# Kernel optimization log

Hardware: AMD Instinct MI355X
Metric: run time of the kernel (lower is better)

Reference implementation:

```python
import jax, jax.numpy as jnp
import numpy as np


def _conv1x1(x, W, b):
    # x: (n, c_in, h, w); W: (c_out, c_in); b: (c_out,)
    return jnp.einsum('nchw,oc->nohw', x, W) + b[None, :, None, None]


def setup_inputs() -> dict:
    key = jax.random.key(0)
    ks = jax.random.split(key, 9)
    n, C, h, w = 2, 256, 64, 64
    Ch = C // 2
    s_in = 0.02
    return {
        'feature': jax.random.normal(ks[0], (n, C, h, w), dtype=jnp.float32),
        'Wq': jax.random.normal(ks[1], (Ch, C), dtype=jnp.float32) * s_in,
        'bq': jax.random.normal(ks[2], (Ch,), dtype=jnp.float32) * s_in,
        'Wk': jax.random.normal(ks[3], (Ch, C), dtype=jnp.float32) * s_in,
        'bk': jax.random.normal(ks[4], (Ch,), dtype=jnp.float32) * s_in,
        'Wv': jax.random.normal(ks[5], (Ch, C), dtype=jnp.float32) * s_in,
        'bv': jax.random.normal(ks[6], (Ch,), dtype=jnp.float32) * s_in,
        'Wm': jax.random.normal(ks[7], (C, Ch), dtype=jnp.float32) * s_in,
        'bm': jax.random.normal(ks[8], (C,), dtype=jnp.float32) * s_in,
    }


def reference(feature, Wq, bq, Wk, bk, Wv, bv, Wm, bm):
    n, C, h, w = feature.shape
    Ch = C // 2
    N = n * h * w
    # 1x1 conv projections, then flatten batch+spatial into one sequence dim
    q = _conv1x1(feature, Wq, bq)  # (n, Ch, h, w)
    k = _conv1x1(feature, Wk, bk)
    v = _conv1x1(feature, Wv, bv)
    # NCHW -> NHWC -> (N, Ch), matching torch transpose(1,2).transpose(2,3).reshape
    q = jnp.transpose(q, (0, 2, 3, 1)).reshape(N, Ch)
    k = jnp.transpose(k, (0, 2, 3, 1)).reshape(N, Ch)
    v = jnp.transpose(v, (0, 2, 3, 1)).reshape(N, Ch)
    # scores = k @ q.T (note: torch code uses k as rows, q.T as cols)
    scores = k @ q.T  # (N, N)
    attn = jax.nn.softmax(scores, axis=-1)
    mask = attn @ v  # (N, Ch)
    mask = mask.reshape(n, h, w, Ch)
    # torch transpose chain (2,3)->(1,2)->(2,3): (n,h,w,Ch) -> (n,Ch,w,h)
    mask = jnp.transpose(mask, (0, 3, 2, 1))
    out = _conv1x1(mask, Wm, bm)  # (n, C, w, h); h==w so residual add is valid
    return out + feature
```

## Files before the change

kernel.cpp:

```cpp
#include <hip/hip_runtime.h>
#include <hip/hip_bf16.h>

#define LOG2E 1.44269504088896340736f

typedef __attribute__((ext_vector_type(8))) short short8;
typedef __attribute__((ext_vector_type(4))) float f32x4;
typedef __attribute__((ext_vector_type(2))) unsigned int uint2v;
typedef __attribute__((ext_vector_type(4))) unsigned int uint4v;
typedef unsigned int u32;

__device__ __forceinline__ short f2bf(float f) {
    unsigned u = __builtin_bit_cast(unsigned, f);
    unsigned r = (u + 0x7FFFu + ((u >> 16) & 1u)) >> 16;
    return (short)r;
}

__device__ __forceinline__ float bf2f(short x) {
    unsigned u = ((unsigned)(unsigned short)x) << 16;
    return __builtin_bit_cast(float, u);
}

__device__ __forceinline__ unsigned cvt_pk_bf16(float lo, float hi) {
    unsigned r;
    asm volatile("v_cvt_pk_bf16_f32 %0, %1, %2" : "=v"(r) : "v"(lo), "v"(hi));
    return r;
}

__device__ __forceinline__ float fexp2(float x) {
    float r;
    asm("v_exp_f32 %0, %1" : "=v"(r) : "v"(x));
    return r;
}

__global__ __launch_bounds__(64) void wprep_kernel(
    const float* __restrict__ Wq, const float* __restrict__ bq,
    const float* __restrict__ Wk, const float* __restrict__ bk,
    const float* __restrict__ Wv, const float* __restrict__ bv,
    const float* __restrict__ Wm,
    short* __restrict__ Wb, float* __restrict__ bqkv, short* __restrict__ Wmb)
{
    const int b = blockIdx.x;
    const int t = threadIdx.x;
    if (b < 384) {
        const int mat = b >> 7, row = b & 127;
        const float* src = (mat == 0 ? Wq : mat == 1 ? Wk : Wv) + (size_t)row * 256;
        const float sc = (mat == 1) ? LOG2E : 1.f;
        float4 v = *(const float4*)(src + t * 4);
        uint2v pk;
        pk.x = cvt_pk_bf16(v.x * sc, v.y * sc);
        pk.y = cvt_pk_bf16(v.z * sc, v.w * sc);
        *(uint2v*)(Wb + (size_t)b * 256 + t * 4) = pk;
    } else if (b == 384) {
        for (int e = t; e < 384; e += 64) {
            const int mat = e >> 7;
            const float* bsrc = (mat == 0 ? bq : mat == 1 ? bk : bv);
            bqkv[e] = bsrc[e & 127] * (mat == 1 ? LOG2E : 1.f);
        }
    } else {
        const int row = b - 385;
        float2 v = *(const float2*)(Wm + (size_t)row * 128 + t * 2);
        *(u32*)(Wmb + (size_t)row * 128 + t * 2) = cvt_pk_bf16(v.x, v.y);
    }
}

__global__ __launch_bounds__(256) void proj_kernel(
    const float* __restrict__ feat, const short* __restrict__ Wb,
    const float* __restrict__ bqkv,
    short* __restrict__ Qb, short* __restrict__ Kb, short* __restrict__ VTp)
{
    __shared__ __align__(16) short Xs[16 * 256];
    __shared__ __align__(16) short VTs[128 * 16];
    const int t = threadIdx.x;
    const int blk = blockIdx.x;
    const int ib = blk * 16;
    const int n = ib >> 12;
    const int hw0 = ib & 4095;

    {
        const int r = t & 15, cg = t >> 4;
        const float* fp = feat + (size_t)n * 1048576 + (size_t)(cg * 16) * 4096 + hw0 + r;
        short8 t0, t1;
        #pragma unroll
        for (int ci = 0; ci < 8; ++ci) {
            t0[ci] = f2bf(fp[(size_t)ci * 4096]);
            t1[ci] = f2bf(fp[(size_t)(ci + 8) * 4096]);
        }
        const int sw = (r & 7) << 2;
        *(short8*)(&Xs[r * 256 + ((cg * 2) ^ sw) * 8]) = t0;
        *(short8*)(&Xs[r * 256 + ((cg * 2 + 1) ^ sw) * 8]) = t1;
    }
    __syncthreads();

    const int lane = t & 63;
    const int w = __builtin_amdgcn_readfirstlane(t >> 6);
    const int l15 = lane & 15;
    const int g = lane >> 4;
    const int o0w = w * 96;

    f32x4 acc[6];
    #pragma unroll
    for (int osub = 0; osub < 6; ++osub)
        acc[osub] = *(const f32x4*)(bqkv + o0w + osub * 16 + 4 * g);

    const short* wbase = Wb + (size_t)(o0w + l15) * 256 + g * 8;
    const int xsw = (l15 & 7) << 2;
    #pragma unroll
    for (int kc = 0; kc < 8; ++kc) {
        short8 xf = *(const short8*)(&Xs[l15 * 256 + (((kc * 4 + g) ^ xsw) * 8)]);
        #pragma unroll
        for (int osub = 0; osub < 6; ++osub) {
            short8 wf = *(const short8*)(wbase + (size_t)osub * 16 * 256 + kc * 32);
            acc[osub] = __builtin_amdgcn_mfma_f32_16x16x32_bf16(wf, xf, acc[osub], 0, 0, 0);
        }
    }

    #pragma unroll
    for (int osub = 0; osub < 6; ++osub) {
        const int o0 = o0w + osub * 16;
        const int mat = o0 >> 7;
        const int col = (o0 & 127) + 4 * g;
        if (mat == 0) {
            uint2v pk;
            pk.x = cvt_pk_bf16(acc[osub][0], acc[osub][1]);
            pk.y = cvt_pk_bf16(acc[osub][2], acc[osub][3]);
            *(uint2v*)(Qb + (size_t)(ib + l15) * 128 + col) = pk;
        } else if (mat == 1) {
            uint2v pk;
            pk.x = cvt_pk_bf16(acc[osub][0], acc[osub][1]);
            pk.y = cvt_pk_bf16(acc[osub][2], acc[osub][3]);
            *(uint2v*)(Kb + (size_t)(ib + l15) * 128 + col) = pk;
        } else {
            #pragma unroll
            for (int reg = 0; reg < 4; ++reg)
                VTs[(col + reg) * 16 + l15] = f2bf(acc[osub][reg]);
        }
    }
    __syncthreads();

    {
        const int o = t >> 1, ih = (t & 1) * 8;
        short8 vv = *(const short8*)(&VTs[o * 16 + ih]);
        const int base32 = ib & ~31;
        const int u = (ib >> 4) & 1;
        const int p0 = 2 * ih + 4 * u;
        uint4v q = __builtin_bit_cast(uint4v, vv);
        uint2v lo; lo.x = q.x; lo.y = q.y;
        uint2v hi; hi.x = q.z; hi.y = q.w;
        *(uint2v*)(VTp + (size_t)o * 8192 + base32 + p0) = lo;
        *(uint2v*)(VTp + (size_t)o * 8192 + base32 + p0 + 8) = hi;
    }
}

__global__ __launch_bounds__(256, 2) void attn_kernel(
    const short* __restrict__ Qb, const short* __restrict__ Kb,
    const short* __restrict__ VTp,
    short* __restrict__ Opart, float* __restrict__ Ssb)
{
    __shared__ __align__(16) char smem[65536];

    const int tid = threadIdx.x;
    const int lane = tid & 63;
    const int w = __builtin_amdgcn_readfirstlane(tid >> 6);
    const int l15 = lane & 15;
    const int g = lane >> 4;
    const int blk = blockIdx.x;
    const int ibX = blk >> 3;
    const int jq  = blk & 7;
    const int iw  = ibX * 128 + w * 32;
    const int j0  = jq * 1024;

    short8 kf[2][4];
    #pragma unroll
    for (int iset = 0; iset < 2; ++iset)
        #pragma unroll
        for (int dcq = 0; dcq < 4; ++dcq)
            kf[iset][dcq] = *(const short8*)(Kb + (size_t)(iw + iset * 16 + l15) * 128 + dcq * 32 + g * 8);

    f32x4 O[2][8];
    #pragma unroll
    for (int iset = 0; iset < 2; ++iset)
        #pragma unroll
        for (int dc = 0; dc < 8; ++dc) O[iset][dc] = (f32x4){0.f, 0.f, 0.f, 0.f};
    float s[2] = {0.f, 0.f};

    const short* srcQ0;
    const short* srcQ1;
    const short* srcV0;
    const short* srcV1;
    {
        int r0 = 4 * w + (lane >> 4), c0 = lane & 15;
        srcQ0 = Qb + (size_t)(j0 + r0) * 128 + (c0 ^ (r0 & 7)) * 8;
        int r1 = 16 + 4 * w + (lane >> 4);
        srcQ1 = Qb + (size_t)(j0 + r1) * 128 + (c0 ^ (r1 & 7)) * 8;
        int d0 = 16 * w + (lane >> 2), c2 = lane & 3;
        srcV0 = VTp + (size_t)d0 * 8192 + j0 + (c2 ^ ((d0 >> 1) & 3)) * 8;
        int d1 = 64 + 16 * w + (lane >> 2);
        srcV1 = VTp + (size_t)d1 * 8192 + j0 + (c2 ^ ((d1 >> 1) & 3)) * 8;
    }

    auto stage = [&](int quarter) {
        char* base = smem + quarter * 16384;
        __builtin_amdgcn_global_load_lds(
            (const __attribute__((address_space(1))) u32*)(const void*)srcQ0,
            (__attribute__((address_space(3))) u32*)(void*)(base + w * 1024), 16, 0, 0);
        __builtin_amdgcn_global_load_lds(
            (const __attribute__((address_space(1))) u32*)(const void*)srcQ1,
            (__attribute__((address_space(3))) u32*)(void*)(base + (4 + w) * 1024), 16, 0, 0);
        __builtin_amdgcn_global_load_lds(
            (const __attribute__((address_space(1))) u32*)(const void*)srcV0,
            (__attribute__((address_space(3))) u32*)(void*)(base + (8 + w) * 1024), 16, 0, 0);
        __builtin_amdgcn_global_load_lds(
            (const __attribute__((address_space(1))) u32*)(const void*)srcV1,
            (__attribute__((address_space(3))) u32*)(void*)(base + (12 + w) * 1024), 16, 0, 0);
        srcQ0 += 32 * 128;
        srcQ1 += 32 * 128;
        srcV0 += 32;
        srcV1 += 32;
    };

    auto compute32 = [&](const char* base) {
        const char* Qt = base;
        const char* Vt = base + 8192;
        const int xs = (l15 & 7) << 4;

        f32x4 sv[2][2];
        #pragma unroll
        for (int jh = 0; jh < 2; ++jh)
            #pragma unroll
            for (int iset = 0; iset < 2; ++iset)
                sv[jh][iset] = (f32x4){-16.f, -16.f, -16.f, -16.f};

        __builtin_amdgcn_s_setprio(1);
        #pragma unroll
        for (int dcq = 0; dcq < 4; ++dcq) {
            short8 qa0 = *(const short8*)(Qt + ((l15 * 256 + dcq * 64 + g * 16) ^ xs));
            short8 qa1 = *(const short8*)(Qt + (((l15 + 16) * 256 + dcq * 64 + g * 16) ^ xs));
            sv[0][0] = __builtin_amdgcn_mfma_f32_16x16x32_bf16(qa0, kf[0][dcq], sv[0][0], 0, 0, 0);
            sv[0][1] = __builtin_amdgcn_mfma_f32_16x16x32_bf16(qa0, kf[1][dcq], sv[0][1], 0, 0, 0);
            sv[1][0] = __builtin_amdgcn_mfma_f32_16x16x32_bf16(qa1, kf[0][dcq], sv[1][0], 0, 0, 0);
            sv[1][1] = __builtin_amdgcn_mfma_f32_16x16x32_bf16(qa1, kf[1][dcq], sv[1][1], 0, 0, 0);
        }
        __builtin_amdgcn_s_setprio(0);

        short8 pf[2];
        #pragma unroll
        for (int iset = 0; iset < 2; ++iset) {
            float p0[4], p1[4], ps = 0.f;
            #pragma unroll
            for (int e = 0; e < 4; ++e) {
                p0[e] = fexp2(sv[0][iset][e]);
                p1[e] = fexp2(sv[1][iset][e]);
                ps += p0[e] + p1[e];
            }
            s[iset] += ps;
            uint4v pk;
            pk.x = cvt_pk_bf16(p0[0], p0[1]);
            pk.y = cvt_pk_bf16(p0[2], p0[3]);
            pk.z = cvt_pk_bf16(p1[0], p1[1]);
            pk.w = cvt_pk_bf16(p1[2], p1[3]);
            pf[iset] = __builtin_bit_cast(short8, pk);
        }

        __builtin_amdgcn_s_setprio(1);
        #pragma unroll
        for (int dc = 0; dc < 8; ++dc) {
            short8 va = *(const short8*)(Vt + (dc * 16 + l15) * 64 + ((g ^ ((l15 >> 1) & 3)) << 4));
            O[0][dc] = __builtin_amdgcn_mfma_f32_16x16x32_bf16(va, pf[0], O[0][dc], 0, 0, 0);
            O[1][dc] = __builtin_amdgcn_mfma_f32_16x16x32_bf16(va, pf[1], O[1][dc], 0, 0, 0);
        }
        __builtin_amdgcn_s_setprio(0);
    };

    stage(0);
    stage(1);
    __syncthreads();
    for (int tt = 0; tt < 32; tt += 2) {
        if (tt + 2 < 32) {
            stage((tt + 2) & 3);
            stage((tt + 3) & 3);
        }
        compute32(smem + (tt & 3) * 16384);
        compute32(smem + ((tt + 1) & 3) * 16384);
        __syncthreads();
    }

    #pragma unroll
    for (int iset = 0; iset < 2; ++iset) {
        const int i = iw + iset * 16 + l15;
        #pragma unroll
        for (int dc = 0; dc < 8; ++dc) {
            uint2v pk;
            pk.x = cvt_pk_bf16(O[iset][dc][0], O[iset][dc][1]);
            pk.y = cvt_pk_bf16(O[iset][dc][2], O[iset][dc][3]);
            *(uint2v*)(Opart + ((size_t)i * 8 + jq) * 128 + dc * 16 + 4 * g) = pk;
        }
        Ssb[(i * 8 + jq) * 4 + g] = s[iset];
    }
}

__global__ __launch_bounds__(256, 4) void epi_kernel(
    const short* __restrict__ Opart, const float* __restrict__ Ssb,
    const short* __restrict__ Wmb, const float* __restrict__ bm,
    const float* __restrict__ feat, float* __restrict__ out)
{
    __shared__ __align__(16) short Ms[16 * 128];
    const int t = threadIdx.x;
    const int blk = blockIdx.x;
    const int yt = blk & 3;
    const int x = (blk >> 2) & 63;
    const int n = blk >> 8;
    const int y0 = yt * 16;

    {
        const int r = t >> 4, c = t & 15;
        const int i = n * 4096 + (y0 + r) * 64 + x;
        float acc8[8] = {0.f, 0.f, 0.f, 0.f, 0.f, 0.f, 0.f, 0.f};
        #pragma unroll
        for (int q = 0; q < 8; ++q) {
            short8 o = *(const short8*)(Opart + ((size_t)i * 8 + q) * 128 + c * 8);
            #pragma unroll
            for (int e = 0; e < 8; ++e) acc8[e] += bf2f(o[e]);
        }
        float2 s2 = *(const float2*)(Ssb + (size_t)i * 32 + c * 2);
        float tp = s2.x + s2.y;
        tp += __shfl_xor(tp, 1);
        tp += __shfl_xor(tp, 2);
        tp += __shfl_xor(tp, 4);
        tp += __shfl_xor(tp, 8);
        const float inv = 1.f / tp;
        uint4v pk;
        pk.x = cvt_pk_bf16(acc8[0] * inv, acc8[1] * inv);
        pk.y = cvt_pk_bf16(acc8[2] * inv, acc8[3] * inv);
        pk.z = cvt_pk_bf16(acc8[4] * inv, acc8[5] * inv);
        pk.w = cvt_pk_bf16(acc8[6] * inv, acc8[7] * inv);
        *(short8*)(&Ms[r * 128 + ((c ^ ((r & 7) << 1)) * 8)]) =
            __builtin_bit_cast(short8, pk);
    }
    __syncthreads();

    const int lane = t & 63;
    const int w = __builtin_amdgcn_readfirstlane(t >> 6);
    const int l15 = lane & 15;
    const int g = lane >> 4;
    const int c0 = w * 64;

    short8 bf[4];
    const int msw = (l15 & 7) << 1;
    #pragma unroll
    for (int dcq = 0; dcq < 4; ++dcq)
        bf[dcq] = *(const short8*)(&Ms[l15 * 128 + (((dcq * 4 + g) ^ msw) * 8)]);

    f32x4 acc[4];
    #pragma unroll
    for (int ct = 0; ct < 4; ++ct)
        acc[ct] = *(const f32x4*)(bm + c0 + ct * 16 + 4 * g);

    const short* wbase = Wmb + (size_t)(c0 + l15) * 128 + g * 8;
    #pragma unroll
    for (int dcq = 0; dcq < 4; ++dcq) {
        #pragma unroll
        for (int ct = 0; ct < 4; ++ct) {
            short8 wf = *(const short8*)(wbase + (size_t)ct * 16 * 128 + dcq * 32);
            acc[ct] = __builtin_amdgcn_mfma_f32_16x16x32_bf16(wf, bf[dcq], acc[ct], 0, 0, 0);
        }
    }

    #pragma unroll
    for (int ct = 0; ct < 4; ++ct) {
        #pragma unroll
        for (int reg = 0; reg < 4; ++reg) {
            const int c = c0 + ct * 16 + 4 * g + reg;
            const size_t oidx = (((size_t)(n * 256 + c) * 64 + x) * 64) + y0 + l15;
            out[oidx] = acc[ct][reg] + feat[oidx];
        }
    }
}

extern "C" void kernel_launch(void* const* d_in, const int* in_sizes, int n_in,
                              void* d_out, int out_size, void* d_ws, size_t ws_size,
                              hipStream_t stream) {
    const float* feat = (const float*)d_in[0];
    const float* Wq = (const float*)d_in[1];
    const float* bq = (const float*)d_in[2];
    const float* Wk = (const float*)d_in[3];
    const float* bk = (const float*)d_in[4];
    const float* Wv = (const float*)d_in[5];
    const float* bv = (const float*)d_in[6];
    const float* Wm = (const float*)d_in[7];
    const float* bm = (const float*)d_in[8];
    float* out = (float*)d_out;

    short* Qb = (short*)d_ws;
    short* Kb = Qb + 8192 * 128;
    short* VTp = Kb + 8192 * 128;
    short* Opart = VTp + 8192 * 128;
    float* Ssb = (float*)(Opart + (size_t)8 * 8192 * 128);
    float* bqkv = Ssb + (size_t)8192 * 32;
    short* Wb = (short*)(bqkv + 384);
    short* Wmb = Wb + 384 * 256;

    hipLaunchKernelGGL(wprep_kernel, dim3(641), dim3(64), 0, stream,
                       Wq, bq, Wk, bk, Wv, bv, Wm, Wb, bqkv, Wmb);
    hipLaunchKernelGGL(proj_kernel, dim3(512), dim3(256), 0, stream,
                       feat, Wb, bqkv, Qb, Kb, VTp);
    hipLaunchKernelGGL(attn_kernel, dim3(512), dim3(256), 0, stream,
                       Qb, Kb, VTp, Opart, Ssb);
    hipLaunchKernelGGL(epi_kernel, dim3(512), dim3(256), 0, stream,
                       Opart, Ssb, Wmb, bm, feat, out);
}
```

Before: 73.89 us.

## Load V fragments directly from global into registers, pre-laid-out per MFMA tile

The projection kernel now writes V in a fragment-ready layout, so each lane of the attention kernel can load its MFMA A-operand with a contiguous 16-byte read. The attention kernel no longer stages V through LDS. It double-buffers V in registers (vA/vB) instead, which halves LDS usage to 32KB. This removes LDS traffic and the V staging work, but adds register pressure and exposes global load latency inside the compute loop.

Result: slower. 76.91 us (+4.1%).

```diff
diff --git a/kernel.cpp b/kernel.cpp
--- a/kernel.cpp
+++ b/kernel.cpp
@@ -66,7 +66,7 @@
 __global__ __launch_bounds__(256) void proj_kernel(
     const float* __restrict__ feat, const short* __restrict__ Wb,
     const float* __restrict__ bqkv,
-    short* __restrict__ Qb, short* __restrict__ Kb, short* __restrict__ VTp)
+    short* __restrict__ Qb, short* __restrict__ Kb, short* __restrict__ VTg)
 {
     __shared__ __align__(16) short Xs[16 * 256];
     __shared__ __align__(16) short VTs[128 * 16];
@@ -140,23 +140,24 @@
     {
         const int o = t >> 1, ih = (t & 1) * 8;
         short8 vv = *(const short8*)(&VTs[o * 16 + ih]);
-        const int base32 = ib & ~31;
+        const int jt = ib >> 5;
         const int u = (ib >> 4) & 1;
-        const int p0 = 2 * ih + 4 * u;
+        const int g0 = ih >> 2;
+        short* vb = VTg + (size_t)jt * 4096 + (o >> 4) * 512 + (o & 15) * 8 + 4 * u;
         uint4v q = __builtin_bit_cast(uint4v, vv);
         uint2v lo; lo.x = q.x; lo.y = q.y;
         uint2v hi; hi.x = q.z; hi.y = q.w;
-        *(uint2v*)(VTp + (size_t)o * 8192 + base32 + p0) = lo;
-        *(uint2v*)(VTp + (size_t)o * 8192 + base32 + p0 + 8) = hi;
+        *(uint2v*)(vb + g0 * 128) = lo;
+        *(uint2v*)(vb + (g0 + 1) * 128) = hi;
     }
 }
 
 __global__ __launch_bounds__(256, 2) void attn_kernel(
     const short* __restrict__ Qb, const short* __restrict__ Kb,
-    const short* __restrict__ VTp,
+    const short* __restrict__ VTg,
     short* __restrict__ Opart, float* __restrict__ Ssb)
 {
-    __shared__ __align__(16) char smem[65536];
+    __shared__ __align__(16) char smem[32768];
 
     const int tid = threadIdx.x;
     const int lane = tid & 63;
@@ -185,42 +186,35 @@
 
     const short* srcQ0;
     const short* srcQ1;
-    const short* srcV0;
-    const short* srcV1;
     {
         int r0 = 4 * w + (lane >> 4), c0 = lane & 15;
         srcQ0 = Qb + (size_t)(j0 + r0) * 128 + (c0 ^ (r0 & 7)) * 8;
         int r1 = 16 + 4 * w + (lane >> 4);
         srcQ1 = Qb + (size_t)(j0 + r1) * 128 + (c0 ^ (r1 & 7)) * 8;
-        int d0 = 16 * w + (lane >> 2), c2 = lane & 3;
-        srcV0 = VTp + (size_t)d0 * 8192 + j0 + (c2 ^ ((d0 >> 1) & 3)) * 8;
-        int d1 = 64 + 16 * w + (lane >> 2);
-        srcV1 = VTp + (size_t)d1 * 8192 + j0 + (c2 ^ ((d1 >> 1) & 3)) * 8;
     }
 
     auto stage = [&](int quarter) {
-        char* base = smem + quarter * 16384;
+        char* base = smem + quarter * 8192;
         __builtin_amdgcn_global_load_lds(
             (const __attribute__((address_space(1))) u32*)(const void*)srcQ0,
             (__attribute__((address_space(3))) u32*)(void*)(base + w * 1024), 16, 0, 0);
         __builtin_amdgcn_global_load_lds(
             (const __attribute__((address_space(1))) u32*)(const void*)srcQ1,
             (__attribute__((address_space(3))) u32*)(void*)(base + (4 + w) * 1024), 16, 0, 0);
-        __builtin_amdgcn_global_load_lds(
-            (const __attribute__((address_space(1))) u32*)(const void*)srcV0,
-            (__attribute__((address_space(3))) u32*)(void*)(base + (8 + w) * 1024), 16, 0, 0);
-        __builtin_amdgcn_global_load_lds(
-            (const __attribute__((address_space(1))) u32*)(const void*)srcV1,
-            (__attribute__((address_space(3))) u32*)(void*)(base + (12 + w) * 1024), 16, 0, 0);
         srcQ0 += 32 * 128;
         srcQ1 += 32 * 128;
-        srcV0 += 32;
-        srcV1 += 32;
     };
 
-    auto compute32 = [&](const char* base) {
-        const char* Qt = base;
-        const char* Vt = base + 8192;
+    const short* vp = VTg + (size_t)(jq * 32) * 4096 + lane * 8;
+    short8 vA[8], vB[8];
+    auto loadV = [&](short8 (&vr)[8]) {
+        #pragma unroll
+        for (int dc = 0; dc < 8; ++dc)
+            vr[dc] = *(const short8*)(vp + dc * 512);
+        vp += 4096;
+    };
+
+    auto compute32 = [&](const char* Qt, const short8 (&vr)[8]) {
         const int xs = (l15 & 7) << 4;
 
         f32x4 sv[2][2];
@@ -264,23 +258,25 @@
         __builtin_amdgcn_s_setprio(1);
         #pragma unroll
         for (int dc = 0; dc < 8; ++dc) {
-            short8 va = *(const short8*)(Vt + (dc * 16 + l15) * 64 + ((g ^ ((l15 >> 1) & 3)) << 4));
-            O[0][dc] = __builtin_amdgcn_mfma_f32_16x16x32_bf16(va, pf[0], O[0][dc], 0, 0, 0);
-            O[1][dc] = __builtin_amdgcn_mfma_f32_16x16x32_bf16(va, pf[1], O[1][dc], 0, 0, 0);
+            O[0][dc] = __builtin_amdgcn_mfma_f32_16x16x32_bf16(vr[dc], pf[0], O[0][dc], 0, 0, 0);
+            O[1][dc] = __builtin_amdgcn_mfma_f32_16x16x32_bf16(vr[dc], pf[1], O[1][dc], 0, 0, 0);
         }
         __builtin_amdgcn_s_setprio(0);
     };
 
     stage(0);
     stage(1);
+    loadV(vA);
     __syncthreads();
     for (int tt = 0; tt < 32; tt += 2) {
         if (tt + 2 < 32) {
             stage((tt + 2) & 3);
             stage((tt + 3) & 3);
         }
-        compute32(smem + (tt & 3) * 16384);
-        compute32(smem + ((tt + 1) & 3) * 16384);
+        loadV(vB);
+        compute32(smem + (tt & 3) * 8192, vA);
+        if (tt + 2 < 32) loadV(vA);
+        compute32(smem + ((tt + 1) & 3) * 8192, vB);
         __syncthreads();
     }
 
@@ -392,8 +388,8 @@
 
     short* Qb = (short*)d_ws;
     short* Kb = Qb + 8192 * 128;
-    short* VTp = Kb + 8192 * 128;
-    short* Opart = VTp + 8192 * 128;
+    short* VTg = Kb + 8192 * 128;
+    short* Opart = VTg + 8192 * 128;
     float* Ssb = (float*)(Opart + (size_t)8 * 8192 * 128);
     float* bqkv = Ssb + (size_t)8192 * 32;
     short* Wb = (short*)(bqkv + 384);
@@ -402,9 +398,9 @@
     hipLaunchKernelGGL(wprep_kernel, dim3(641), dim3(64), 0, stream,
                        Wq, bq, Wk, bk, Wv, bv, Wm, Wb, bqkv, Wmb);
     hipLaunchKernelGGL(proj_kernel, dim3(512), dim3(256), 0, stream,
-                       feat, Wb, bqkv, Qb, Kb, VTp);
+                       feat, Wb, bqkv, Qb, Kb, VTg);
     hipLaunchKernelGGL(attn_kernel, dim3(512), dim3(256), 0, stream,
-                       Qb, Kb, VTp, Opart, Ssb);
+                       Qb, Kb, VTg, Opart, Ssb);
     hipLaunchKernelGGL(epi_kernel, dim3(512), dim3(256), 0, stream,
                        Opart, Ssb, Wmb, bm, feat, out);
 }
```

## Switch attention to 32x32x16 MFMA with fragment-native Q/K/V layouts

Applied to the files above, without the earlier changes.

The projection kernel now writes Q, K and V in a pre-tiled layout that matches the operand fragments of the 32x32x16 bf16 MFMA. The attention kernel then replaces its 16x16x32 MFMAs with fewer, larger 32x32 MFMAs, and its LDS reads become straight lane-contiguous loads with no XOR swizzle. The aim is to cut instruction count and LDS addressing overhead per tile. The row-sum partials shrink from four per row to two, and the epilogue indexing changes to match. The risk is LDS bank conflicts, since the swizzle is gone, and higher accumulator register pressure.

Result: no change. 73.84 us (-0.1%).

```diff
diff --git a/kernel.cpp b/kernel.cpp
--- a/kernel.cpp
+++ b/kernel.cpp
@@ -5,6 +5,7 @@
 
 typedef __attribute__((ext_vector_type(8))) short short8;
 typedef __attribute__((ext_vector_type(4))) float f32x4;
+typedef __attribute__((ext_vector_type(16))) float f32x16;
 typedef __attribute__((ext_vector_type(2))) unsigned int uint2v;
 typedef __attribute__((ext_vector_type(4))) unsigned int uint4v;
 typedef unsigned int u32;
@@ -66,7 +67,7 @@
 __global__ __launch_bounds__(256) void proj_kernel(
     const float* __restrict__ feat, const short* __restrict__ Wb,
     const float* __restrict__ bqkv,
-    short* __restrict__ Qb, short* __restrict__ Kb, short* __restrict__ VTp)
+    short* __restrict__ Qg, short* __restrict__ Kg, short* __restrict__ Vg)
 {
     __shared__ __align__(16) short Xs[16 * 256];
     __shared__ __align__(16) short VTs[128 * 16];
@@ -118,18 +119,20 @@
     for (int osub = 0; osub < 6; ++osub) {
         const int o0 = o0w + osub * 16;
         const int mat = o0 >> 7;
-        const int col = (o0 & 127) + 4 * g;
-        if (mat == 0) {
+        if (mat < 2) {
+            const int ch0 = (o0 & 127) + 4 * g;
+            const int kc = ch0 >> 4;
+            const int hh = (ch0 >> 3) & 1;
+            const int e0 = ch0 & 7;
+            const int j = ib + l15;
+            short* dst = (mat == 0 ? Qg : Kg)
+                + (size_t)(j >> 5) * 4096 + kc * 512 + ((j & 31) + 32 * hh) * 8 + e0;
             uint2v pk;
             pk.x = cvt_pk_bf16(acc[osub][0], acc[osub][1]);
             pk.y = cvt_pk_bf16(acc[osub][2], acc[osub][3]);
-            *(uint2v*)(Qb + (size_t)(ib + l15) * 128 + col) = pk;
-        } else if (mat == 1) {
-            uint2v pk;
-            pk.x = cvt_pk_bf16(acc[osub][0], acc[osub][1]);
-            pk.y = cvt_pk_bf16(acc[osub][2], acc[osub][3]);
-            *(uint2v*)(Kb + (size_t)(ib + l15) * 128 + col) = pk;
+            *(uint2v*)dst = pk;
         } else {
+            const int col = (o0 & 127) + 4 * g;
             #pragma unroll
             for (int reg = 0; reg < 4; ++reg)
                 VTs[(col + reg) * 16 + l15] = f2bf(acc[osub][reg]);
@@ -140,20 +143,21 @@
     {
         const int o = t >> 1, ih = (t & 1) * 8;
         short8 vv = *(const short8*)(&VTs[o * 16 + ih]);
-        const int base32 = ib & ~31;
-        const int u = (ib >> 4) & 1;
-        const int p0 = 2 * ih + 4 * u;
+        const int jt = ib >> 5;
+        const int nn = (ib >> 4) & 1;
+        short* vb = Vg + (size_t)jt * 4096 + (o >> 5) * 1024 + nn * 512
+                      + (o & 31) * 8 + (ih >> 1);
         uint4v q = __builtin_bit_cast(uint4v, vv);
         uint2v lo; lo.x = q.x; lo.y = q.y;
         uint2v hi; hi.x = q.z; hi.y = q.w;
-        *(uint2v*)(VTp + (size_t)o * 8192 + base32 + p0) = lo;
-        *(uint2v*)(VTp + (size_t)o * 8192 + base32 + p0 + 8) = hi;
+        *(uint2v*)(vb) = lo;
+        *(uint2v*)(vb + 256) = hi;
     }
 }
 
 __global__ __launch_bounds__(256, 2) void attn_kernel(
-    const short* __restrict__ Qb, const short* __restrict__ Kb,
-    const short* __restrict__ VTp,
+    const short* __restrict__ Qg, const short* __restrict__ Kg,
+    const short* __restrict__ Vg,
     short* __restrict__ Opart, float* __restrict__ Ssb)
 {
     __shared__ __align__(16) char smem[65536];
@@ -161,112 +165,87 @@
     const int tid = threadIdx.x;
     const int lane = tid & 63;
     const int w = __builtin_amdgcn_readfirstlane(tid >> 6);
-    const int l15 = lane & 15;
-    const int g = lane >> 4;
+    const int l31 = lane & 31;
+    const int h = lane >> 5;
     const int blk = blockIdx.x;
     const int ibX = blk >> 3;
     const int jq  = blk & 7;
     const int iw  = ibX * 128 + w * 32;
     const int j0  = jq * 1024;
 
-    short8 kf[2][4];
-    #pragma unroll
-    for (int iset = 0; iset < 2; ++iset)
-        #pragma unroll
-        for (int dcq = 0; dcq < 4; ++dcq)
-            kf[iset][dcq] = *(const short8*)(Kb + (size_t)(iw + iset * 16 + l15) * 128 + dcq * 32 + g * 8);
-
-    f32x4 O[2][8];
-    #pragma unroll
-    for (int iset = 0; iset < 2; ++iset)
-        #pragma unroll
-        for (int dc = 0; dc < 8; ++dc) O[iset][dc] = (f32x4){0.f, 0.f, 0.f, 0.f};
-    float s[2] = {0.f, 0.f};
-
-    const short* srcQ0;
-    const short* srcQ1;
-    const short* srcV0;
-    const short* srcV1;
-    {
-        int r0 = 4 * w + (lane >> 4), c0 = lane & 15;
-        srcQ0 = Qb + (size_t)(j0 + r0) * 128 + (c0 ^ (r0 & 7)) * 8;
-        int r1 = 16 + 4 * w + (lane >> 4);
-        srcQ1 = Qb + (size_t)(j0 + r1) * 128 + (c0 ^ (r1 & 7)) * 8;
-        int d0 = 16 * w + (lane >> 2), c2 = lane & 3;
-        srcV0 = VTp + (size_t)d0 * 8192 + j0 + (c2 ^ ((d0 >> 1) & 3)) * 8;
-        int d1 = 64 + 16 * w + (lane >> 2);
-        srcV1 = VTp + (size_t)d1 * 8192 + j0 + (c2 ^ ((d1 >> 1) & 3)) * 8;
-    }
+    short8 kf[8];
+    {
+        const short* kp = Kg + (size_t)(iw >> 5) * 4096 + lane * 8;
+        #pragma unroll
+        for (int kc = 0; kc < 8; ++kc) kf[kc] = *(const short8*)(kp + kc * 512);
+    }
+
+    f32x16 O[4];
+    #pragma unroll
+    for (int dc = 0; dc < 4; ++dc)
+        #pragma unroll
+        for (int e = 0; e < 16; ++e) O[dc][e] = 0.f;
+    float s = 0.f;
+
+    const short* srcQ = Qg + (size_t)(j0 >> 5) * 4096 + w * 512 + lane * 8;
+    const short* srcV = Vg + (size_t)(j0 >> 5) * 4096 + w * 512 + lane * 8;
 
     auto stage = [&](int quarter) {
         char* base = smem + quarter * 16384;
         __builtin_amdgcn_global_load_lds(
-            (const __attribute__((address_space(1))) u32*)(const void*)srcQ0,
+            (const __attribute__((address_space(1))) u32*)(const void*)srcQ,
             (__attribute__((address_space(3))) u32*)(void*)(base + w * 1024), 16, 0, 0);
         __builtin_amdgcn_global_load_lds(
-            (const __attribute__((address_space(1))) u32*)(const void*)srcQ1,
+            (const __attribute__((address_space(1))) u32*)(const void*)(srcQ + 2048),
             (__attribute__((address_space(3))) u32*)(void*)(base + (4 + w) * 1024), 16, 0, 0);
         __builtin_amdgcn_global_load_lds(
-            (const __attribute__((address_space(1))) u32*)(const void*)srcV0,
-            (__attribute__((address_space(3))) u32*)(void*)(base + (8 + w) * 1024), 16, 0, 0);
+            (const __attribute__((address_space(1))) u32*)(const void*)srcV,
+            (__attribute__((address_space(3))) u32*)(void*)(base + 8192 + w * 1024), 16, 0, 0);
         __builtin_amdgcn_global_load_lds(
-            (const __attribute__((address_space(1))) u32*)(const void*)srcV1,
-            (__attribute__((address_space(3))) u32*)(void*)(base + (12 + w) * 1024), 16, 0, 0);
-        srcQ0 += 32 * 128;
-        srcQ1 += 32 * 128;
-        srcV0 += 32;
-        srcV1 += 32;
+            (const __attribute__((address_space(1))) u32*)(const void*)(srcV + 2048),
+            (__attribute__((address_space(3))) u32*)(void*)(base + 8192 + (4 + w) * 1024), 16, 0, 0);
+        srcQ += 4096;
+        srcV += 4096;
     };
 
     auto compute32 = [&](const char* base) {
         const char* Qt = base;
         const char* Vt = base + 8192;
-        const int xs = (l15 & 7) << 4;
-
-        f32x4 sv[2][2];
-        #pragma unroll
-        for (int jh = 0; jh < 2; ++jh)
-            #pragma unroll
-            for (int iset = 0; iset < 2; ++iset)
-                sv[jh][iset] = (f32x4){-16.f, -16.f, -16.f, -16.f};
+
+        f32x16 sv;
+        #pragma unroll
+        for (int e = 0; e < 16; ++e) sv[e] = -16.f;
 
         __builtin_amdgcn_s_setprio(1);
         #pragma unroll
-        for (int dcq = 0; dcq < 4; ++dcq) {
-            short8 qa0 = *(const short8*)(Qt + ((l15 * 256 + dcq * 64 + g * 16) ^ xs));
-            short8 qa1 = *(const short8*)(Qt + (((l15 + 16) * 256 + dcq * 64 + g * 16) ^ xs));
-            sv[0][0] = __builtin_amdgcn_mfma_f32_16x16x32_bf16(qa0, kf[0][dcq], sv[0][0], 0, 0, 0);
-            sv[0][1] = __builtin_amdgcn_mfma_f32_16x16x32_bf16(qa0, kf[1][dcq], sv[0][1], 0, 0, 0);
-            sv[1][0] = __builtin_amdgcn_mfma_f32_16x16x32_bf16(qa1, kf[0][dcq], sv[1][0], 0, 0, 0);
-            sv[1][1] = __builtin_amdgcn_mfma_f32_16x16x32_bf16(qa1, kf[1][dcq], sv[1][1], 0, 0, 0);
+        for (int kc = 0; kc < 8; ++kc) {
+            short8 qa = *(const short8*)(Qt + kc * 1024 + lane * 16);
+            sv = __builtin_amdgcn_mfma_f32_32x32x16_bf16(qa, kf[kc], sv, 0, 0, 0);
         }
         __builtin_amdgcn_s_setprio(0);
 
-        short8 pf[2];
-        #pragma unroll
-        for (int iset = 0; iset < 2; ++iset) {
-            float p0[4], p1[4], ps = 0.f;
-            #pragma unroll
-            for (int e = 0; e < 4; ++e) {
-                p0[e] = fexp2(sv[0][iset][e]);
-                p1[e] = fexp2(sv[1][iset][e]);
-                ps += p0[e] + p1[e];
-            }
-            s[iset] += ps;
-            uint4v pk;
-            pk.x = cvt_pk_bf16(p0[0], p0[1]);
-            pk.y = cvt_pk_bf16(p0[2], p0[3]);
-            pk.z = cvt_pk_bf16(p1[0], p1[1]);
-            pk.w = cvt_pk_bf16(p1[2], p1[3]);
-            pf[iset] = __builtin_bit_cast(short8, pk);
+        float p[16], ps = 0.f;
+        #pragma unroll
+        for (int r = 0; r < 16; ++r) { p[r] = fexp2(sv[r]); ps += p[r]; }
+        s += ps;
+        short8 pf0, pf1;
+        {
+            uint4v a, b;
+            a.x = cvt_pk_bf16(p[0], p[1]);  a.y = cvt_pk_bf16(p[2], p[3]);
+            a.z = cvt_pk_bf16(p[4], p[5]);  a.w = cvt_pk_bf16(p[6], p[7]);
+            b.x = cvt_pk_bf16(p[8], p[9]);  b.y = cvt_pk_bf16(p[10], p[11]);
+            b.z = cvt_pk_bf16(p[12], p[13]); b.w = cvt_pk_bf16(p[14], p[15]);
+            pf0 = __builtin_bit_cast(short8, a);
+            pf1 = __builtin_bit_cast(short8, b);
         }
 
         __builtin_amdgcn_s_setprio(1);
         #pragma unroll
-        for (int dc = 0; dc < 8; ++dc) {
-            short8 va = *(const short8*)(Vt + (dc * 16 + l15) * 64 + ((g ^ ((l15 >> 1) & 3)) << 4));
-            O[0][dc] = __builtin_amdgcn_mfma_f32_16x16x32_bf16(va, pf[0], O[0][dc], 0, 0, 0);
-            O[1][dc] = __builtin_amdgcn_mfma_f32_16x16x32_bf16(va, pf[1], O[1][dc], 0, 0, 0);
+        for (int dc = 0; dc < 4; ++dc) {
+            short8 va0 = *(const short8*)(Vt + dc * 2048 + lane * 16);
+            short8 va1 = *(const short8*)(Vt + dc * 2048 + 1024 + lane * 16);
+            O[dc] = __builtin_amdgcn_mfma_f32_32x32x16_bf16(va0, pf0, O[dc], 0, 0, 0);
+            O[dc] = __builtin_amdgcn_mfma_f32_32x32x16_bf16(va1, pf1, O[dc], 0, 0, 0);
         }
         __builtin_amdgcn_s_setprio(0);
     };
@@ -284,17 +263,20 @@
         __syncthreads();
     }
 
-    #pragma unroll
-    for (int iset = 0; iset < 2; ++iset) {
-        const int i = iw + iset * 16 + l15;
-        #pragma unroll
-        for (int dc = 0; dc < 8; ++dc) {
-            uint2v pk;
-            pk.x = cvt_pk_bf16(O[iset][dc][0], O[iset][dc][1]);
-            pk.y = cvt_pk_bf16(O[iset][dc][2], O[iset][dc][3]);
-            *(uint2v*)(Opart + ((size_t)i * 8 + jq) * 128 + dc * 16 + 4 * g) = pk;
-        }
-        Ssb[(i * 8 + jq) * 4 + g] = s[iset];
+    {
+        const int i = iw + l31;
+        short* op = Opart + ((size_t)i * 8 + jq) * 128;
+        #pragma unroll
+        for (int dc = 0; dc < 4; ++dc) {
+            #pragma unroll
+            for (int q4 = 0; q4 < 4; ++q4) {
+                uint2v pk;
+                pk.x = cvt_pk_bf16(O[dc][4 * q4 + 0], O[dc][4 * q4 + 1]);
+                pk.y = cvt_pk_bf16(O[dc][4 * q4 + 2], O[dc][4 * q4 + 3]);
+                *(uint2v*)(op + dc * 32 + q4 * 8 + 4 * h) = pk;
+            }
+        }
+        Ssb[((size_t)i * 8 + jq) * 2 + h] = s;
     }
 }
 
@@ -321,8 +303,7 @@
             #pragma unroll
             for (int e = 0; e < 8; ++e) acc8[e] += bf2f(o[e]);
         }
-        float2 s2 = *(const float2*)(Ssb + (size_t)i * 32 + c * 2);
-        float tp = s2.x + s2.y;
+        float tp = Ssb[(size_t)i * 16 + c];
         tp += __shfl_xor(tp, 1);
         tp += __shfl_xor(tp, 2);
         tp += __shfl_xor(tp, 4);
@@ -390,21 +371,21 @@
     const float* bm = (const float*)d_in[8];
     float* out = (float*)d_out;
 
-    short* Qb = (short*)d_ws;
-    short* Kb = Qb + 8192 * 128;
-    short* VTp = Kb + 8192 * 128;
-    short* Opart = VTp + 8192 * 128;
+    short* Qg = (short*)d_ws;
+    short* Kg = Qg + 8192 * 128;
+    short* Vg = Kg + 8192 * 128;
+    short* Opart = Vg + 8192 * 128;
     float* Ssb = (float*)(Opart + (size_t)8 * 8192 * 128);
-    float* bqkv = Ssb + (size_t)8192 * 32;
+    float* bqkv = Ssb + (size_t)8192 * 16;
     short* Wb = (short*)(bqkv + 384);
     short* Wmb = Wb + 384 * 256;
 
     hipLaunchKernelGGL(wprep_kernel, dim3(641), dim3(64), 0, stream,
                        Wq, bq, Wk, bk, Wv, bv, Wm, Wb, bqkv, Wmb);
     hipLaunchKernelGGL(proj_kernel, dim3(512), dim3(256), 0, stream,
-                       feat, Wb, bqkv, Qb, Kb, VTp);
+                       feat, Wb, bqkv, Qg, Kg, Vg);
     hipLaunchKernelGGL(attn_kernel, dim3(512), dim3(256), 0, stream,
-                       Qb, Kb, VTp, Opart, Ssb);
+                       Qg, Kg, Vg, Opart, Ssb);
     hipLaunchKernelGGL(epi_kernel, dim3(512), dim3(256), 0, stream,
                        Opart, Ssb, Wmb, bm, feat, out);
 }
```
